# Optimization experiments

Hardware: AMD Instinct MI355X
Metric: run time of the kernel (lower is better)

## Reference

```python
import jax, jax.numpy as jnp
import numpy as np

B, N, D, L = 8, 2048, 1024, 128


def setup_inputs() -> dict:
    key = jax.random.key(0)
    ks = jax.random.split(key, 8)
    return {
        "e_i_t_minus_1": jax.random.normal(ks[0], (B, D), dtype=jnp.float32),
        "e_j_t": jax.random.normal(ks[1], (B, N, D), dtype=jnp.float32),
        "imp_j_t": jax.random.uniform(ks[2], (B, N), dtype=jnp.float32),
        "R_lk": jax.random.normal(ks[3], (L, D), dtype=jnp.float32),
        "W_q": jax.random.normal(ks[4], (D, D), dtype=jnp.float32) * (D ** -0.5),
        "W_k": jax.random.normal(ks[5], (D, D), dtype=jnp.float32) * (D ** -0.5),
        "W_v": jax.random.normal(ks[6], (D, D), dtype=jnp.float32) * (D ** -0.5),
        "omega": jax.random.normal(ks[7], (D,), dtype=jnp.float32),
    }


def reference(e_i_t_minus_1, e_j_t, imp_j_t, R_lk, W_q, W_k, W_v, omega):
    # torch nn.Linear(x) = x @ W.T  (weights stored [out, in])
    q_i = jnp.einsum('bd,ed->be', e_i_t_minus_1, W_q)[:, None, :]   # [B,1,D]
    k_j = jnp.einsum('bnd,ed->bne', e_j_t, W_k)                      # [B,N,D]
    sigma = jnp.einsum('bnd,d->bn', jnp.tanh(q_i + k_j), omega)      # [B,N]
    exp_sigma = jnp.exp(sigma)
    sum_exp = jnp.sum(exp_sigma, axis=1, keepdims=True)              # [B,1]
    a_ij = imp_j_t * exp_sigma / (sum_exp + 1e-9)                    # [B,N]
    v_j = jnp.einsum('bnd,ed->bne', e_j_t, W_v)                      # [B,N,D]
    A = jnp.einsum('bn,bnd->bd', a_ij, v_j)                          # [B,D]
    # R_lk[l,d] * a_ij[b,n] * v_j[b,n,d], summed over n -> [B,L,D]
    A_lk = jnp.einsum('bn,bnd,ld->bld', a_ij, v_j, R_lk)             # [B,L,D]
    A_l = A                                                          # identical math in source
    return (A, A_lk, A_l)
```

## Files before the change

### kernel.cpp

```cpp
#include <hip/hip_runtime.h>
#include <hip/hip_bf16.h>
#include <math.h>

#define BB 8
#define NN 2048
#define DD 1024
#define LL 128
#define MM (BB*NN)

typedef _Float16 half8 __attribute__((ext_vector_type(8)));
typedef _Float16 half4 __attribute__((ext_vector_type(4)));
typedef __attribute__((ext_vector_type(4))) float floatx4;

__device__ __forceinline__ void glds16(const void* g, void* l) {
    __builtin_amdgcn_global_load_lds(
        (const __attribute__((address_space(1))) unsigned int*)g,
        (__attribute__((address_space(3))) unsigned int*)l, 16, 0, 0);
}

__device__ __forceinline__ float ftanh(float x) {
    float e = __expf(2.0f * x);
    return 1.0f - 2.0f * __builtin_amdgcn_rcpf(e + 1.0f);
}

__global__ __launch_bounds__(256) void prep_kernel(const float* __restrict__ e_j,
                                                   _Float16* __restrict__ eh,
                                                   const float* __restrict__ Wk,
                                                   _Float16* __restrict__ wh,
                                                   const float* __restrict__ e_i,
                                                   const float* __restrict__ Wq,
                                                   float* __restrict__ q) {
    __shared__ float us[BB][DD];
    int blk = blockIdx.x;
    int tid = threadIdx.x;
    if (blk < 8192) {
        int i = blk * 256 + tid;
        const float4* xp = (const float4*)e_j + (size_t)i * 2;
        float4 v0 = xp[0], v1 = xp[1];
        half8 h;
        h[0] = (_Float16)v0.x; h[1] = (_Float16)v0.y;
        h[2] = (_Float16)v0.z; h[3] = (_Float16)v0.w;
        h[4] = (_Float16)v1.x; h[5] = (_Float16)v1.y;
        h[6] = (_Float16)v1.z; h[7] = (_Float16)v1.w;
        *(half8*)(eh + (size_t)i * 8) = h;
    } else if (blk < 8704) {
        int i = (blk - 8192) * 256 + tid;
        const float4* xp = (const float4*)Wk + (size_t)i * 2;
        float4 v0 = xp[0], v1 = xp[1];
        half8 h;
        h[0] = (_Float16)v0.x; h[1] = (_Float16)v0.y;
        h[2] = (_Float16)v0.z; h[3] = (_Float16)v0.w;
        h[4] = (_Float16)v1.x; h[5] = (_Float16)v1.y;
        h[6] = (_Float16)v1.z; h[7] = (_Float16)v1.w;
        *(half8*)(wh + (size_t)i * 8) = h;
    } else {
        for (int i = tid; i < BB * DD / 4; i += 256)
            ((float4*)&us[0][0])[i] = ((const float4*)e_i)[i];
        __syncthreads();
        int w = tid >> 6, lane = tid & 63;
        int d = (blk - 8704) * 4 + w;
        float acc[8] = {0.f, 0.f, 0.f, 0.f, 0.f, 0.f, 0.f, 0.f};
        for (int e0 = 0; e0 < DD; e0 += 256) {
            float4 wv = *(const float4*)&Wq[(size_t)d * DD + e0 + lane * 4];
            #pragma unroll
            for (int r = 0; r < 8; ++r) {
                float4 uv = *(const float4*)&us[r][e0 + lane * 4];
                acc[r] += wv.x * uv.x + wv.y * uv.y + wv.z * uv.z + wv.w * uv.w;
            }
        }
        #pragma unroll
        for (int r = 0; r < 8; ++r) {
            float s = acc[r];
            #pragma unroll
            for (int off = 32; off; off >>= 1) s += __shfl_down(s, off, 64);
            if (lane == 0) q[r * DD + d] = s;
        }
    }
}

__global__ __launch_bounds__(512, 2) void sigma256(const _Float16* __restrict__ eh,
                                                   const _Float16* __restrict__ wh,
                                                   const float* __restrict__ q,
                                                   const float* __restrict__ omega,
                                                   float* __restrict__ sig_part)
{
    __shared__ _Float16 As[2][2][128][64];
    __shared__ _Float16 Bs[2][2][128][64];

    const int tid  = threadIdx.x;
    const int lane = tid & 63;
    const int wid  = tid >> 6;
    const int wm   = wid >> 2;
    const int wn   = wid & 3;
    const int c15  = lane & 15, quad = lane >> 4;

    const int wgid   = (blockIdx.x & 7) * 32 + (blockIdx.x >> 3);
    const int colBlk = wgid >> 6;
    const int rowBlk = wgid & 63;
    const int row0   = rowBlk * 256;
    const int col0   = colBlk * 256;
    const int b      = row0 / NN;

    const int l3  = lane >> 3;
    const int qst = ((lane & 7) ^ l3) * 8;
    const _Float16* gA = eh + (size_t)(row0 + wid * 16 + l3) * DD + qst;
    const _Float16* gB = wh + (size_t)(col0 + wid * 16 + l3) * DD + qst;
    char* const ldsA = (char*)&As[0][0][0][0] + wid * 2048;
    char* const ldsB = (char*)&Bs[0][0][0][0] + wid * 2048;

#define STG_A(kt, hf, s) do { \
    glds16(gA + (size_t)(hf) * 128 * DD + (kt) * 64,          ldsA + (s) * 32768 + (hf) * 16384); \
    glds16(gA + (size_t)(hf) * 128 * DD + (kt) * 64 + 8 * DD, ldsA + (s) * 32768 + (hf) * 16384 + 1024); } while (0)
#define STG_B(kt, hf, s) do { \
    glds16(gB + (size_t)(hf) * 128 * DD + (kt) * 64,          ldsB + (s) * 32768 + (hf) * 16384); \
    glds16(gB + (size_t)(hf) * 128 * DD + (kt) * 64 + 8 * DD, ldsB + (s) * 32768 + (hf) * 16384 + 1024); } while (0)

    const int swz = c15 & 7;
    const int q0  = (quad ^ swz) << 4;
    const int q1  = ((4 + quad) ^ swz) << 4;
    const char* const afp = (const char*)&As[0][0][0][0] + wm * 16384 + c15 * 128;
    const char* const bfp = (const char*)&Bs[0][0][0][0] + (wn >> 1) * 16384
                            + ((wn & 1) * 64 + c15) * 128;
#define FA(s, m, ks) (*(const half8*)(afp + (s) * 32768 + (m) * 2048 + ((ks) ? q1 : q0)))
#define FB(s, n, ks) (*(const half8*)(bfp + (s) * 32768 + (n) * 2048 + ((ks) ? q1 : q0)))

    floatx4 acc[8][4];
    #pragma unroll
    for (int m = 0; m < 8; ++m)
        #pragma unroll
        for (int n = 0; n < 4; ++n) acc[m][n] = (floatx4){0.f, 0.f, 0.f, 0.f};

    half8 a[8], bl[4], bh[4];

#define BARx()  __builtin_amdgcn_s_barrier()
#define SBARx() __builtin_amdgcn_sched_barrier(0)
#define LGKM0() asm volatile("s_waitcnt lgkmcnt(0)" ::: "memory")
#define MFMA16(MB, NB, BARR) \
    __builtin_amdgcn_s_setprio(1); \
    _Pragma("unroll") for (int m_ = 0; m_ < 4; ++m_) \
    _Pragma("unroll") for (int n_ = 0; n_ < 2; ++n_) \
    _Pragma("unroll") for (int ks_ = 0; ks_ < 2; ++ks_) \
        acc[(MB) + m_][(NB) + n_] = __builtin_amdgcn_mfma_f32_16x16x32_f16( \
            a[m_ * 2 + ks_], BARR[n_ * 2 + ks_], acc[(MB) + m_][(NB) + n_], 0, 0, 0); \
    __builtin_amdgcn_s_setprio(0);

#define PH_A(s, STAGE) \
    _Pragma("unroll") for (int m_ = 0; m_ < 4; ++m_) { a[m_*2] = FA(s, m_, 0); a[m_*2+1] = FA(s, m_, 1); } \
    _Pragma("unroll") for (int n_ = 0; n_ < 2; ++n_) { bl[n_*2] = FB(s, n_, 0); bl[n_*2+1] = FB(s, n_, 1); } \
    STAGE; SBARx(); BARx(); LGKM0(); SBARx(); MFMA16(0, 0, bl) BARx();
#define PH_B(s, STAGE) \
    _Pragma("unroll") for (int n_ = 0; n_ < 2; ++n_) { bh[n_*2] = FB(s, 2+n_, 0); bh[n_*2+1] = FB(s, 2+n_, 1); } \
    STAGE; SBARx(); BARx(); LGKM0(); SBARx(); MFMA16(0, 2, bh) BARx();
#define PH_C(s, STAGE) \
    _Pragma("unroll") for (int m_ = 0; m_ < 4; ++m_) { a[m_*2] = FA(s, 4+m_, 0); a[m_*2+1] = FA(s, 4+m_, 1); } \
    STAGE; SBARx(); BARx(); LGKM0(); SBARx(); MFMA16(4, 0, bl) BARx();
#define PH_D(s, STAGE, VMW) \
    STAGE; SBARx(); BARx(); LGKM0(); SBARx(); MFMA16(4, 2, bh) \
    asm volatile("s_waitcnt vmcnt(" VMW ")" ::: "memory"); BARx();

    STG_A(0, 0, 0); STG_A(0, 1, 0); STG_B(0, 0, 0); STG_B(0, 1, 0);
    STG_B(1, 0, 1); STG_B(1, 1, 1);
    asm volatile("s_waitcnt vmcnt(4)" ::: "memory");
    BARx();

    for (int i = 0; i < 7; ++i) {
        const int k1 = 2 * i + 1, k2 = 2 * i + 2, k3 = 2 * i + 3;
        PH_A(0, STG_A(k1, 0, 1))
        PH_B(0, STG_A(k1, 1, 1))
        PH_C(0, STG_B(k2, 0, 0))
        PH_D(0, STG_B(k2, 1, 0), "4")
        PH_A(1, STG_A(k2, 0, 0))
        PH_B(1, STG_A(k2, 1, 0))
        PH_C(1, STG_B(k3, 0, 1))
        PH_D(1, STG_B(k3, 1, 1), "4")
    }
    PH_A(0, STG_A(15, 0, 1))
    PH_B(0, STG_A(15, 1, 1))
    PH_C(0, ((void)0))
    PH_D(0, ((void)0), "0")
    PH_A(1, ((void)0))
    PH_B(1, ((void)0))
    PH_C(1, ((void)0))
    PH_D(1, ((void)0), "0")

#undef PH_A
#undef PH_B
#undef PH_C
#undef PH_D
#undef MFMA16
#undef FA
#undef FB
#undef STG_A
#undef STG_B

    float part[8][4];
    #pragma unroll
    for (int m = 0; m < 8; ++m)
        #pragma unroll
        for (int r = 0; r < 4; ++r) part[m][r] = 0.f;

    #pragma unroll
    for (int n = 0; n < 4; ++n) {
        int col = col0 + wn * 64 + n * 16 + c15;
        float qv = q[b * DD + col];
        float om = omega[col];
        #pragma unroll
        for (int m = 0; m < 8; ++m)
            #pragma unroll
            for (int r = 0; r < 4; ++r)
                part[m][r] += ftanh(acc[m][n][r] + qv) * om;
    }

    float (*red)[4] = (float(*)[4])&As[0][0][0][0];
    #pragma unroll
    for (int m = 0; m < 8; ++m)
        #pragma unroll
        for (int r = 0; r < 4; ++r) {
            float s = part[m][r];
            s += __shfl_xor(s, 1, 64);
            s += __shfl_xor(s, 2, 64);
            s += __shfl_xor(s, 4, 64);
            s += __shfl_xor(s, 8, 64);
            if (c15 == 0) red[wm * 128 + m * 16 + quad * 4 + r][wn] = s;
        }
    __syncthreads();
    if (tid < 256)
        sig_part[(size_t)colBlk * MM + row0 + tid] =
            red[tid][0] + red[tid][1] + red[tid][2] + red[tid][3];
}

__global__ __launch_bounds__(256) void softmax_k(const float* __restrict__ sig_part,
                                                 const float* __restrict__ imp,
                                                 float* __restrict__ a_ij) {
    int b = blockIdx.x >> 3, slice = blockIdx.x & 7;
    int tid = threadIdx.x;
    __shared__ float red[256];
    float sv[8];
    float m = -1e30f;
    #pragma unroll
    for (int p = 0; p < 8; ++p) {
        int n = p * 256 + tid;
        float s = 0.f;
        #pragma unroll
        for (int db = 0; db < 4; ++db) s += sig_part[db * MM + b * NN + n];
        sv[p] = s;
        m = fmaxf(m, s);
    }
    red[tid] = m; __syncthreads();
    for (int off = 128; off; off >>= 1) {
        if (tid < off) red[tid] = fmaxf(red[tid], red[tid + off]);
        __syncthreads();
    }
    m = red[0]; __syncthreads();
    float sum = 0.f;
    #pragma unroll
    for (int p = 0; p < 8; ++p) sum += expf(sv[p] - m);
    red[tid] = sum; __syncthreads();
    for (int off = 128; off; off >>= 1) {
        if (tid < off) red[tid] += red[tid + off];
        __syncthreads();
    }
    float inv = 1.f / (red[0] + 1e-9f * expf(-m));
    int n = slice * 256 + tid;
    a_ij[b * NN + n] = imp[b * NN + n] * expf(sv[slice] - m) * inv;
}

__global__ __launch_bounds__(256) void u_kernel(const float* __restrict__ a_ij,
                                                const _Float16* __restrict__ eh,
                                                float* __restrict__ u_part) {
    int b = blockIdx.x >> 7, nc = blockIdx.x & 127;
    int t = threadIdx.x;
    float4 acc = {0.f, 0.f, 0.f, 0.f};
    const _Float16* base = eh + ((size_t)(b * NN + nc * 16)) * DD + t * 4;
    const float* ap = a_ij + b * NN + nc * 16;
    #pragma unroll
    for (int n = 0; n < 16; ++n) {
        float a = ap[n];
        half4 v = *(const half4*)(base + (size_t)n * DD);
        acc.x += a * (float)v[0]; acc.y += a * (float)v[1];
        acc.z += a * (float)v[2]; acc.w += a * (float)v[3];
    }
    *(float4*)(u_part + ((size_t)nc * BB + b) * DD + t * 4) = acc;
}

__global__ __launch_bounds__(256) void ureduce(const float* __restrict__ u_part,
                                               float* __restrict__ u) {
    int i = blockIdx.x * 256 + threadIdx.x;
    float s = 0.f;
    #pragma unroll 8
    for (int nc = 0; nc < 128; ++nc) s += u_part[(size_t)nc * BB * DD + i];
    u[i] = s;
}

__global__ __launch_bounds__(256) void rowdot8(const float* __restrict__ X,
                                               const float* __restrict__ W,
                                               float* __restrict__ out) {
    __shared__ float us[BB][DD];
    int tid = threadIdx.x;
    for (int i = tid; i < BB * DD / 4; i += 256)
        ((float4*)&us[0][0])[i] = ((const float4*)X)[i];
    __syncthreads();
    int w = tid >> 6, lane = tid & 63;
    int d = blockIdx.x * 4 + w;
    float acc[8] = {0.f, 0.f, 0.f, 0.f, 0.f, 0.f, 0.f, 0.f};
    for (int e0 = 0; e0 < DD; e0 += 256) {
        float4 wv = *(const float4*)&W[(size_t)d * DD + e0 + lane * 4];
        #pragma unroll
        for (int r = 0; r < 8; ++r) {
            float4 uv = *(const float4*)&us[r][e0 + lane * 4];
            acc[r] += wv.x * uv.x + wv.y * uv.y + wv.z * uv.z + wv.w * uv.w;
        }
    }
    #pragma unroll
    for (int r = 0; r < 8; ++r) {
        float s = acc[r];
        #pragma unroll
        for (int off = 32; off; off >>= 1) s += __shfl_down(s, off, 64);
        if (lane == 0) out[r * DD + d] = s;
    }
}

__global__ __launch_bounds__(256) void out_kernel(const float* __restrict__ A,
                                                  const float* __restrict__ Rlk,
                                                  float* __restrict__ out) {
    int i = blockIdx.x * 256 + threadIdx.x;
    int d = i & (DD - 1);
    int l = (i >> 10) & (LL - 1);
    int b = i >> 17;
    out[BB * DD + i] = A[b * DD + d] * Rlk[l * DD + d];
    if (i < BB * DD) {
        out[i] = A[i];
        out[BB * DD + BB * LL * DD + i] = A[i];
    }
}

extern "C" void kernel_launch(void* const* d_in, const int* in_sizes, int n_in,
                              void* d_out, int out_size, void* d_ws, size_t ws_size,
                              hipStream_t stream) {
    const float* e_i   = (const float*)d_in[0];
    const float* e_j   = (const float*)d_in[1];
    const float* imp   = (const float*)d_in[2];
    const float* Rlk   = (const float*)d_in[3];
    const float* Wq    = (const float*)d_in[4];
    const float* Wk    = (const float*)d_in[5];
    const float* Wv    = (const float*)d_in[6];
    const float* omega = (const float*)d_in[7];
    float* out = (float*)d_out;
    float* ws  = (float*)d_ws;

    float* q    = ws;
    float* sigp = ws + 8192;
    float* a_ij = ws + 139264;
    float* u    = ws + 155648;
    _Float16* eh = (_Float16*)(ws + 172032);
    _Float16* wh = eh + (size_t)MM * DD;
    float* u_part = (float*)(wh + (size_t)DD * DD);

    prep_kernel<<<8960, 256, 0, stream>>>(e_j, eh, Wk, wh, e_i, Wq, q);

    sigma256<<<dim3(256), 512, 0, stream>>>(eh, wh, q, omega, sigp);

    softmax_k<<<64, 256, 0, stream>>>(sigp, imp, a_ij);

    u_kernel<<<1024, 256, 0, stream>>>(a_ij, eh, u_part);
    ureduce<<<32, 256, 0, stream>>>(u_part, u);

    rowdot8<<<256, 256, 0, stream>>>(u, Wv, a_ij);

    out_kernel<<<(BB * LL * DD) / 256, 256, 0, stream>>>(a_ij, Rlk, out);
}
```

Measured before the change: 185.0 us.

## Fuse softmax into weighted sum, merge projection with output, re-pipeline GEMM

The sigma GEMM main loop is rescheduled so the LDS fragment reads for the next phase are issued before the MFMAs of the current phase, using double A registers and partial lgkmcnt waits in place of full drains. Softmax is fused into the weighted-sum kernel: each block recomputes the row max and sum itself and accumulates u with atomics, so the a_ij round trip, the partial buffer and the reduce kernel go away. The Wv projection and the A_lk broadcast output are merged into one kernel. The costs are that every block redundantly recomputes the full softmax statistics, and that float atomics make the sum order nondeterministic.

```diff
diff --git a/kernel.cpp b/kernel.cpp
--- a/kernel.cpp
+++ b/kernel.cpp
@@ -29,7 +29,8 @@
                                                    _Float16* __restrict__ wh,
                                                    const float* __restrict__ e_i,
                                                    const float* __restrict__ Wq,
-                                                   float* __restrict__ q) {
+                                                   float* __restrict__ q,
+                                                   float* __restrict__ u) {
     __shared__ float us[BB][DD];
     int blk = blockIdx.x;
     int tid = threadIdx.x;
@@ -53,7 +54,7 @@
         h[4] = (_Float16)v1.x; h[5] = (_Float16)v1.y;
         h[6] = (_Float16)v1.z; h[7] = (_Float16)v1.w;
         *(half8*)(wh + (size_t)i * 8) = h;
-    } else {
+    } else if (blk < 8960) {
         for (int i = tid; i < BB * DD / 4; i += 256)
             ((float4*)&us[0][0])[i] = ((const float4*)e_i)[i];
         __syncthreads();
@@ -75,6 +76,8 @@
             for (int off = 32; off; off >>= 1) s += __shfl_down(s, off, 64);
             if (lane == 0) q[r * DD + d] = s;
         }
+    } else {
+        u[(blk - 8960) * 256 + tid] = 0.f;
     }
 }
 
@@ -114,6 +117,8 @@
 #define STG_B(kt, hf, s) do { \
     glds16(gB + (size_t)(hf) * 128 * DD + (kt) * 64,          ldsB + (s) * 32768 + (hf) * 16384); \
     glds16(gB + (size_t)(hf) * 128 * DD + (kt) * 64 + 8 * DD, ldsB + (s) * 32768 + (hf) * 16384 + 1024); } while (0)
+#define STG_P5(k2) do { STG_B(k2, 1, 0); STG_A(k2, 0, 0); } while (0)
+#define STG_P8(k3) do { STG_B(k3, 0, 1); STG_B(k3, 1, 1); } while (0)
 
     const int swz = c15 & 7;
     const int q0  = (quad ^ swz) << 4;
@@ -130,68 +135,84 @@
         #pragma unroll
         for (int n = 0; n < 4; ++n) acc[m][n] = (floatx4){0.f, 0.f, 0.f, 0.f};
 
-    half8 a[8], bl[4], bh[4];
+    half8 a1[8], a2[8], bl[4], bh[4];
 
 #define BARx()  __builtin_amdgcn_s_barrier()
 #define SBARx() __builtin_amdgcn_sched_barrier(0)
-#define LGKM0() asm volatile("s_waitcnt lgkmcnt(0)" ::: "memory")
-#define MFMA16(MB, NB, BARR) \
+#define WT4  asm volatile("s_waitcnt lgkmcnt(4)" ::: "memory")
+#define WT8  asm volatile("s_waitcnt lgkmcnt(8)" ::: "memory")
+#define WT0  asm volatile("s_waitcnt lgkmcnt(0)" ::: "memory")
+#define VMC2 asm volatile("s_waitcnt vmcnt(2)" ::: "memory")
+#define VMC4 asm volatile("s_waitcnt vmcnt(4)" ::: "memory")
+#define VMC0 asm volatile("s_waitcnt vmcnt(0)" ::: "memory")
+#define NOPX ((void)0)
+
+#define RD_F1(s) \
+    _Pragma("unroll") for (int m_ = 0; m_ < 4; ++m_) { a1[m_*2] = FA(s, m_, 0); a1[m_*2+1] = FA(s, m_, 1); } \
+    _Pragma("unroll") for (int n_ = 0; n_ < 2; ++n_) { bl[n_*2] = FB(s, n_, 0); bl[n_*2+1] = FB(s, n_, 1); }
+#define RD_F2(s) \
+    _Pragma("unroll") for (int n_ = 0; n_ < 2; ++n_) { bh[n_*2] = FB(s, 2+n_, 0); bh[n_*2+1] = FB(s, 2+n_, 1); }
+#define RD_F3(s) \
+    _Pragma("unroll") for (int m_ = 0; m_ < 4; ++m_) { a2[m_*2] = FA(s, 4+m_, 0); a2[m_*2+1] = FA(s, 4+m_, 1); }
+
+#define MFM(AR, BR, MB, NB) do { \
     __builtin_amdgcn_s_setprio(1); \
     _Pragma("unroll") for (int m_ = 0; m_ < 4; ++m_) \
     _Pragma("unroll") for (int n_ = 0; n_ < 2; ++n_) \
     _Pragma("unroll") for (int ks_ = 0; ks_ < 2; ++ks_) \
-        acc[(MB) + m_][(NB) + n_] = __builtin_amdgcn_mfma_f32_16x16x32_f16( \
-            a[m_ * 2 + ks_], BARR[n_ * 2 + ks_], acc[(MB) + m_][(NB) + n_], 0, 0, 0); \
-    __builtin_amdgcn_s_setprio(0);
-
-#define PH_A(s, STAGE) \
-    _Pragma("unroll") for (int m_ = 0; m_ < 4; ++m_) { a[m_*2] = FA(s, m_, 0); a[m_*2+1] = FA(s, m_, 1); } \
-    _Pragma("unroll") for (int n_ = 0; n_ < 2; ++n_) { bl[n_*2] = FB(s, n_, 0); bl[n_*2+1] = FB(s, n_, 1); } \
-    STAGE; SBARx(); BARx(); LGKM0(); SBARx(); MFMA16(0, 0, bl) BARx();
-#define PH_B(s, STAGE) \
-    _Pragma("unroll") for (int n_ = 0; n_ < 2; ++n_) { bh[n_*2] = FB(s, 2+n_, 0); bh[n_*2+1] = FB(s, 2+n_, 1); } \
-    STAGE; SBARx(); BARx(); LGKM0(); SBARx(); MFMA16(0, 2, bh) BARx();
-#define PH_C(s, STAGE) \
-    _Pragma("unroll") for (int m_ = 0; m_ < 4; ++m_) { a[m_*2] = FA(s, 4+m_, 0); a[m_*2+1] = FA(s, 4+m_, 1); } \
-    STAGE; SBARx(); BARx(); LGKM0(); SBARx(); MFMA16(4, 0, bl) BARx();
-#define PH_D(s, STAGE, VMW) \
-    STAGE; SBARx(); BARx(); LGKM0(); SBARx(); MFMA16(4, 2, bh) \
-    asm volatile("s_waitcnt vmcnt(" VMW ")" ::: "memory"); BARx();
+        acc[(MB)+m_][(NB)+n_] = __builtin_amdgcn_mfma_f32_16x16x32_f16( \
+            AR[m_*2+ks_], BR[n_*2+ks_], acc[(MB)+m_][(NB)+n_], 0, 0, 0); \
+    __builtin_amdgcn_s_setprio(0); } while (0)
+
+#define PHASE(RD, ST, WT, MM_, VM) do { RD; ST; SBARx(); BARx(); WT; SBARx(); MM_; VM; BARx(); } while (0)
 
     STG_A(0, 0, 0); STG_A(0, 1, 0); STG_B(0, 0, 0); STG_B(0, 1, 0);
     STG_B(1, 0, 1); STG_B(1, 1, 1);
-    asm volatile("s_waitcnt vmcnt(4)" ::: "memory");
+    VMC4;
     BARx();
 
-    for (int i = 0; i < 7; ++i) {
+    PHASE(RD_F1(0), STG_A(1, 0, 1), NOPX, NOPX,              NOPX);
+    PHASE(RD_F2(0), STG_A(1, 1, 1), WT4,  MFM(a1, bl, 0, 0), NOPX);
+    PHASE(RD_F3(0), NOPX,           WT8,  MFM(a1, bh, 0, 2), NOPX);
+    PHASE(NOPX,     STG_B(2, 0, 0), WT0,  MFM(a2, bl, 4, 0), VMC2);
+    PHASE(RD_F1(1), STG_P5(2),      NOPX, MFM(a2, bh, 4, 2), NOPX);
+    PHASE(RD_F2(1), STG_A(2, 1, 0), WT4,  MFM(a1, bl, 0, 0), NOPX);
+    PHASE(RD_F3(1), NOPX,           WT8,  MFM(a1, bh, 0, 2), NOPX);
+    PHASE(NOPX,     STG_P8(3),      WT0,  MFM(a2, bl, 4, 0), VMC4);
+
+    for (int i = 1; i < 7; ++i) {
         const int k1 = 2 * i + 1, k2 = 2 * i + 2, k3 = 2 * i + 3;
-        PH_A(0, STG_A(k1, 0, 1))
-        PH_B(0, STG_A(k1, 1, 1))
-        PH_C(0, STG_B(k2, 0, 0))
-        PH_D(0, STG_B(k2, 1, 0), "4")
-        PH_A(1, STG_A(k2, 0, 0))
-        PH_B(1, STG_A(k2, 1, 0))
-        PH_C(1, STG_B(k3, 0, 1))
-        PH_D(1, STG_B(k3, 1, 1), "4")
-    }
-    PH_A(0, STG_A(15, 0, 1))
-    PH_B(0, STG_A(15, 1, 1))
-    PH_C(0, ((void)0))
-    PH_D(0, ((void)0), "0")
-    PH_A(1, ((void)0))
-    PH_B(1, ((void)0))
-    PH_C(1, ((void)0))
-    PH_D(1, ((void)0), "0")
-
-#undef PH_A
-#undef PH_B
-#undef PH_C
-#undef PH_D
-#undef MFMA16
+        PHASE(RD_F1(0), STG_A(k1, 0, 1), NOPX, MFM(a2, bh, 4, 2), NOPX);
+        PHASE(RD_F2(0), STG_A(k1, 1, 1), WT4,  MFM(a1, bl, 0, 0), NOPX);
+        PHASE(RD_F3(0), NOPX,            WT8,  MFM(a1, bh, 0, 2), NOPX);
+        PHASE(NOPX,     STG_B(k2, 0, 0), WT0,  MFM(a2, bl, 4, 0), VMC2);
+        PHASE(RD_F1(1), STG_P5(k2),      NOPX, MFM(a2, bh, 4, 2), NOPX);
+        PHASE(RD_F2(1), STG_A(k2, 1, 0), WT4,  MFM(a1, bl, 0, 0), NOPX);
+        PHASE(RD_F3(1), NOPX,            WT8,  MFM(a1, bh, 0, 2), NOPX);
+        PHASE(NOPX,     STG_P8(k3),      WT0,  MFM(a2, bl, 4, 0), VMC4);
+    }
+
+    PHASE(RD_F1(0), STG_A(15, 0, 1), NOPX, MFM(a2, bh, 4, 2), NOPX);
+    PHASE(RD_F2(0), STG_A(15, 1, 1), WT4,  MFM(a1, bl, 0, 0), NOPX);
+    PHASE(RD_F3(0), NOPX,            WT8,  MFM(a1, bh, 0, 2), NOPX);
+    PHASE(NOPX,     NOPX,            WT0,  MFM(a2, bl, 4, 0), VMC0);
+    PHASE(RD_F1(1), NOPX,            NOPX, MFM(a2, bh, 4, 2), NOPX);
+    PHASE(RD_F2(1), NOPX,            WT4,  MFM(a1, bl, 0, 0), NOPX);
+    PHASE(RD_F3(1), NOPX,            WT8,  MFM(a1, bh, 0, 2), NOPX);
+    PHASE(NOPX,     NOPX,            WT0,  MFM(a2, bl, 4, 0), NOPX);
+    MFM(a2, bh, 4, 2);
+
+#undef PHASE
+#undef MFM
+#undef RD_F1
+#undef RD_F2
+#undef RD_F3
 #undef FA
 #undef FB
 #undef STG_A
 #undef STG_B
+#undef STG_P5
+#undef STG_P8
 
     float part[8][4];
     #pragma unroll
@@ -229,21 +250,23 @@
             red[tid][0] + red[tid][1] + red[tid][2] + red[tid][3];
 }
 
-__global__ __launch_bounds__(256) void softmax_k(const float* __restrict__ sig_part,
+__global__ __launch_bounds__(256) void su_kernel(const float* __restrict__ sig_part,
                                                  const float* __restrict__ imp,
-                                                 float* __restrict__ a_ij) {
-    int b = blockIdx.x >> 3, slice = blockIdx.x & 7;
+                                                 const _Float16* __restrict__ eh,
+                                                 float* __restrict__ u) {
+    int b = blockIdx.x >> 7, nc = blockIdx.x & 127;
     int tid = threadIdx.x;
     __shared__ float red[256];
-    float sv[8];
-    float m = -1e30f;
+    __shared__ float a_s[16];
+    float m = -1e30f, sum;
+    float svv[8];
     #pragma unroll
     for (int p = 0; p < 8; ++p) {
         int n = p * 256 + tid;
         float s = 0.f;
         #pragma unroll
         for (int db = 0; db < 4; ++db) s += sig_part[db * MM + b * NN + n];
-        sv[p] = s;
+        svv[p] = s;
         m = fmaxf(m, s);
     }
     red[tid] = m; __syncthreads();
@@ -252,85 +275,89 @@
         __syncthreads();
     }
     m = red[0]; __syncthreads();
-    float sum = 0.f;
-    #pragma unroll
-    for (int p = 0; p < 8; ++p) sum += expf(sv[p] - m);
+    sum = 0.f;
+    #pragma unroll
+    for (int p = 0; p < 8; ++p) sum += expf(svv[p] - m);
     red[tid] = sum; __syncthreads();
     for (int off = 128; off; off >>= 1) {
         if (tid < off) red[tid] += red[tid + off];
         __syncthreads();
     }
     float inv = 1.f / (red[0] + 1e-9f * expf(-m));
-    int n = slice * 256 + tid;
-    a_ij[b * NN + n] = imp[b * NN + n] * expf(sv[slice] - m) * inv;
-}
-
-__global__ __launch_bounds__(256) void u_kernel(const float* __restrict__ a_ij,
-                                                const _Float16* __restrict__ eh,
-                                                float* __restrict__ u_part) {
-    int b = blockIdx.x >> 7, nc = blockIdx.x & 127;
-    int t = threadIdx.x;
+    if (tid < 16) {
+        int n = nc * 16 + tid;
+        float s = 0.f;
+        #pragma unroll
+        for (int db = 0; db < 4; ++db) s += sig_part[db * MM + b * NN + n];
+        a_s[tid] = imp[b * NN + n] * expf(s - m) * inv;
+    }
+    __syncthreads();
     float4 acc = {0.f, 0.f, 0.f, 0.f};
-    const _Float16* base = eh + ((size_t)(b * NN + nc * 16)) * DD + t * 4;
-    const float* ap = a_ij + b * NN + nc * 16;
+    const _Float16* base = eh + ((size_t)(b * NN + nc * 16)) * DD + tid * 4;
     #pragma unroll
     for (int n = 0; n < 16; ++n) {
-        float a = ap[n];
+        float a = a_s[n];
         half4 v = *(const half4*)(base + (size_t)n * DD);
         acc.x += a * (float)v[0]; acc.y += a * (float)v[1];
         acc.z += a * (float)v[2]; acc.w += a * (float)v[3];
     }
-    *(float4*)(u_part + ((size_t)nc * BB + b) * DD + t * 4) = acc;
-}
-
-__global__ __launch_bounds__(256) void ureduce(const float* __restrict__ u_part,
-                                               float* __restrict__ u) {
-    int i = blockIdx.x * 256 + threadIdx.x;
-    float s = 0.f;
-    #pragma unroll 8
-    for (int nc = 0; nc < 128; ++nc) s += u_part[(size_t)nc * BB * DD + i];
-    u[i] = s;
-}
-
-__global__ __launch_bounds__(256) void rowdot8(const float* __restrict__ X,
-                                               const float* __restrict__ W,
-                                               float* __restrict__ out) {
+    float* up = u + (size_t)b * DD + tid * 4;
+    atomicAdd(up + 0, acc.x);
+    atomicAdd(up + 1, acc.y);
+    atomicAdd(up + 2, acc.z);
+    atomicAdd(up + 3, acc.w);
+}
+
+__global__ __launch_bounds__(256) void fin_kernel(const float* __restrict__ u,
+                                                  const float* __restrict__ Wv,
+                                                  const float* __restrict__ Rlk,
+                                                  float* __restrict__ out) {
     __shared__ float us[BB][DD];
+    __shared__ float As[BB][8];
     int tid = threadIdx.x;
     for (int i = tid; i < BB * DD / 4; i += 256)
-        ((float4*)&us[0][0])[i] = ((const float4*)X)[i];
+        ((float4*)&us[0][0])[i] = ((const float4*)u)[i];
     __syncthreads();
     int w = tid >> 6, lane = tid & 63;
-    int d = blockIdx.x * 4 + w;
-    float acc[8] = {0.f, 0.f, 0.f, 0.f, 0.f, 0.f, 0.f, 0.f};
-    for (int e0 = 0; e0 < DD; e0 += 256) {
-        float4 wv = *(const float4*)&W[(size_t)d * DD + e0 + lane * 4];
+    #pragma unroll
+    for (int dd = 0; dd < 2; ++dd) {
+        int dl = w * 2 + dd;
+        int d = blockIdx.x * 8 + dl;
+        float acc[8] = {0.f, 0.f, 0.f, 0.f, 0.f, 0.f, 0.f, 0.f};
+        for (int e0 = 0; e0 < DD; e0 += 256) {
+            float4 wv = *(const float4*)&Wv[(size_t)d * DD + e0 + lane * 4];
+            #pragma unroll
+            for (int r = 0; r < 8; ++r) {
+                float4 uv = *(const float4*)&us[r][e0 + lane * 4];
+                acc[r] += wv.x * uv.x + wv.y * uv.y + wv.z * uv.z + wv.w * uv.w;
+            }
+        }
         #pragma unroll
         for (int r = 0; r < 8; ++r) {
-            float4 uv = *(const float4*)&us[r][e0 + lane * 4];
-            acc[r] += wv.x * uv.x + wv.y * uv.y + wv.z * uv.z + wv.w * uv.w;
-        }
-    }
-    #pragma unroll
-    for (int r = 0; r < 8; ++r) {
-        float s = acc[r];
-        #pragma unroll
-        for (int off = 32; off; off >>= 1) s += __shfl_down(s, off, 64);
-        if (lane == 0) out[r * DD + d] = s;
-    }
-}
-
-__global__ __launch_bounds__(256) void out_kernel(const float* __restrict__ A,
-                                                  const float* __restrict__ Rlk,
-                                                  float* __restrict__ out) {
-    int i = blockIdx.x * 256 + threadIdx.x;
-    int d = i & (DD - 1);
-    int l = (i >> 10) & (LL - 1);
-    int b = i >> 17;
-    out[BB * DD + i] = A[b * DD + d] * Rlk[l * DD + d];
-    if (i < BB * DD) {
-        out[i] = A[i];
-        out[BB * DD + BB * LL * DD + i] = A[i];
+            float s = acc[r];
+            #pragma unroll
+            for (int off = 32; off; off >>= 1) s += __shfl_down(s, off, 64);
+            if (lane == 0) {
+                As[r][dl] = s;
+                out[r * DD + d] = s;
+                out[BB * DD + BB * LL * DD + r * DD + d] = s;
+            }
+        }
+    }
+    __syncthreads();
+    int k8 = blockIdx.x * 8;
+    for (int c = tid; c < BB * LL; c += 256) {
+        int bb = c >> 7, l = c & 127;
+        float4 r0 = *(const float4*)&Rlk[(size_t)l * DD + k8];
+        float4 r1 = *(const float4*)&Rlk[(size_t)l * DD + k8 + 4];
+        float4 o0, o1;
+        o0.x = As[bb][0] * r0.x; o0.y = As[bb][1] * r0.y;
+        o0.z = As[bb][2] * r0.z; o0.w = As[bb][3] * r0.w;
+        o1.x = As[bb][4] * r1.x; o1.y = As[bb][5] * r1.y;
+        o1.z = As[bb][6] * r1.z; o1.w = As[bb][7] * r1.w;
+        size_t o = (size_t)BB * DD + (size_t)bb * LL * DD + (size_t)l * DD + k8;
+        *(float4*)&out[o]     = o0;
+        *(float4*)&out[o + 4] = o1;
     }
 }
 
@@ -350,22 +377,15 @@
 
     float* q    = ws;
     float* sigp = ws + 8192;
-    float* a_ij = ws + 139264;
     float* u    = ws + 155648;
     _Float16* eh = (_Float16*)(ws + 172032);
     _Float16* wh = eh + (size_t)MM * DD;
-    float* u_part = (float*)(wh + (size_t)DD * DD);
-
-    prep_kernel<<<8960, 256, 0, stream>>>(e_j, eh, Wk, wh, e_i, Wq, q);
+
+    prep_kernel<<<8992, 256, 0, stream>>>(e_j, eh, Wk, wh, e_i, Wq, q, u);
 
     sigma256<<<dim3(256), 512, 0, stream>>>(eh, wh, q, omega, sigp);
 
-    softmax_k<<<64, 256, 0, stream>>>(sigp, imp, a_ij);
-
-    u_kernel<<<1024, 256, 0, stream>>>(a_ij, eh, u_part);
-    ureduce<<<32, 256, 0, stream>>>(u_part, u);
-
-    rowdot8<<<256, 256, 0, stream>>>(u, Wv, a_ij);
-
-    out_kernel<<<(BB * LL * DD) / 256, 256, 0, stream>>>(a_ij, Rlk, out);
-}
+    su_kernel<<<1024, 256, 0, stream>>>(sigp, imp, eh, u);
+
+    fin_kernel<<<128, 256, 0, stream>>>(u, Wv, Rlk, out);
+}
```

Result: slower. 214.6 us (+16.0%).
